# Performance work log

Measured on AMD Instinct MI355X. Metric: run time of the kernel, lower is better.

## Reference

```python
import jax, jax.numpy as jnp
import numpy as np

INPUT_SIZE = 64
HIDDEN = 128


def setup_inputs() -> dict:
    key = jax.random.key(0)
    ks = jax.random.split(key, 10)
    B, T, I, H = 512, 1024, INPUT_SIZE, HIDDEN
    s_ih = 1.0 / np.sqrt(H)
    inp = {
        "x": jax.random.normal(ks[0], (B, T, I), dtype=jnp.float32),
        # PyTorch nn.LSTM params, gate order (i, f, g, o)
        "W_ih": jax.random.uniform(ks[1], (4 * H, I), jnp.float32, -s_ih, s_ih),
        "W_hh": jax.random.uniform(ks[2], (4 * H, H), jnp.float32, -s_ih, s_ih),
        "b_ih": jax.random.uniform(ks[3], (4 * H,), jnp.float32, -s_ih, s_ih),
        "b_hh": jax.random.uniform(ks[4], (4 * H,), jnp.float32, -s_ih, s_ih),
        # fc1: 128 -> 256, fc2: 256 -> 1 (PyTorch Linear init bounds)
        "W1": jax.random.uniform(ks[5], (256, H), jnp.float32, -s_ih, s_ih),
        "b1": jax.random.uniform(ks[6], (256,), jnp.float32, -s_ih, s_ih),
        "W2": jax.random.uniform(ks[7], (1, 256), jnp.float32, -1.0 / 16, 1.0 / 16),
        "b2": jax.random.uniform(ks[8], (1,), jnp.float32, -1.0 / 16, 1.0 / 16),
    }
    return inp


def _lstm_last_hidden(x, W_ih, W_hh, b_ih, b_hh):
    B, T, I = x.shape
    H = W_hh.shape[1]
    # Precompute input projection for all timesteps in one big GEMM: [T, B, 4H]
    x_proj = jnp.einsum("bti,gi->tbg", x, W_ih) + (b_ih + b_hh)

    def step(carry, xp_t):
        h, c = carry
        gates = xp_t + h @ W_hh.T  # [B, 4H]
        i_g, f_g, g_g, o_g = jnp.split(gates, 4, axis=-1)
        i_g = jax.nn.sigmoid(i_g)
        f_g = jax.nn.sigmoid(f_g)
        g_g = jnp.tanh(g_g)
        o_g = jax.nn.sigmoid(o_g)
        c = f_g * c + i_g * g_g
        h = o_g * jnp.tanh(c)
        return (h, c), None

    h0 = jnp.zeros((B, H), dtype=x.dtype)
    c0 = jnp.zeros((B, H), dtype=x.dtype)
    (h_T, _), _ = jax.lax.scan(step, (h0, c0), x_proj)
    return h_T  # [B, H], equals output at last timestep


def reference(x, W_ih, W_hh, b_ih, b_hh, W1, b1, W2, b2):
    h_last = _lstm_last_hidden(x, W_ih, W_hh, b_ih, b_hh)  # x[:, -1, :] of LSTM outputs
    y = h_last @ W1.T + b1   # fc1 (no activation in original)
    y = y @ W2.T + b2        # fc2 -> [B, 1]
    return y
```

## Files before the change

### kernel.cpp

```cpp
#include <hip/hip_runtime.h>


#define T_STEPS 1024
#define ISZ 64
#define HSZ 128
#define ZSZ (ISZ + HSZ)
#define G4 512
#define BCHUNK 2
#define NTH 512
#define CLEN 48
#define NGATE 4

__device__ __forceinline__ float fast_sigmoid(float x) {
    return 1.0f / (1.0f + __expf(-x));
}

__device__ __forceinline__ float fast_tanh(float x) {
    float xc = fminf(fmaxf(x, -15.0f), 15.0f);
    float u = __expf(2.0f * xc);
    return (u - 1.0f) / (u + 1.0f);
}

__device__ __forceinline__ float quad_reduce(float v) {
    int t = __builtin_amdgcn_mov_dpp(__float_as_int(v), 0xB1, 0xF, 0xF, true);
    v += __int_as_float(t);
    t = __builtin_amdgcn_mov_dpp(__float_as_int(v), 0x4E, 0xF, 0xF, true);
    v += __int_as_float(t);
    return v;
}

__global__ __launch_bounds__(NTH, 2)
void lstm_fused_kernel(const float* __restrict__ x,
                       const float* __restrict__ W_ih,
                       const float* __restrict__ W_hh,
                       const float* __restrict__ b_ih,
                       const float* __restrict__ b_hh,
                       const float* __restrict__ W1,
                       const float* __restrict__ b1,
                       const float* __restrict__ W2,
                       const float* __restrict__ b2,
                       float* __restrict__ out)
{
    __shared__ __align__(16) float zbuf[BCHUNK][ZSZ];
    __shared__ __align__(16) float gbuf[BCHUNK][G4];
    __shared__ float red[BCHUNK][4];

    const int tid = threadIdx.x;
    const int b0 = blockIdx.x * BCHUNK;
    const int c  = tid & 3;
    const int qg = tid >> 2;

    float wt[NGATE][CLEN];
    #pragma unroll
    for (int i = 0; i < NGATE; ++i) {
        const int g = qg * 4 + i;
        const float* pih = W_ih + (size_t)g * ISZ;
        const float* phh = W_hh + (size_t)g * HSZ;
        #pragma unroll
        for (int k = 0; k < CLEN; ++k) {
            const int col = c * CLEN + k;
            const float* p = (col < ISZ) ? (pih + col) : (phh + (col - ISZ));
            wt[i][k] = *p;
        }
    }
    const float bias = b_ih[tid] + b_hh[tid];

    if (tid < BCHUNK * HSZ) zbuf[tid >> 7][ISZ + (tid & 127)] = 0.0f;
    if (tid >= 256 && tid < 256 + BCHUNK * ISZ) {
        int l = tid - 256;
        zbuf[l >> 6][l & 63] =
            x[((size_t)(b0 + (l >> 6)) * T_STEPS + 0) * ISZ + (l & 63)];
    }
    float c0 = 0.0f, c1 = 0.0f;
    __syncthreads();

    const int gsel = tid >> 7;

    for (int t = 0; t < T_STEPS; ++t) {
        float xpre = 0.0f;
        const bool pf = (tid >= 128) && (tid < 256) && (t + 1 < T_STEPS);
        if (pf) {
            int l = tid - 128;
            xpre = x[((size_t)(b0 + (l >> 6)) * T_STEPS + (t + 1)) * ISZ + (l & 63)];
        }

        float a[NGATE][2];
        #pragma unroll
        for (int i = 0; i < NGATE; ++i) { a[i][0] = 0.0f; a[i][1] = 0.0f; }
        {
            const float4* z0 = reinterpret_cast<const float4*>(zbuf[0]) + c * (CLEN / 4);
            const float4* z1 = reinterpret_cast<const float4*>(zbuf[1]) + c * (CLEN / 4);
            #pragma unroll
            for (int k = 0; k < CLEN / 4; ++k) {
                float4 u = z0[k];
                float4 v = z1[k];
                #pragma unroll
                for (int i = 0; i < NGATE; ++i) {
                    a[i][0] = fmaf(wt[i][4*k  ], u.x, a[i][0]);
                    a[i][0] = fmaf(wt[i][4*k+1], u.y, a[i][0]);
                    a[i][0] = fmaf(wt[i][4*k+2], u.z, a[i][0]);
                    a[i][0] = fmaf(wt[i][4*k+3], u.w, a[i][0]);
                    a[i][1] = fmaf(wt[i][4*k  ], v.x, a[i][1]);
                    a[i][1] = fmaf(wt[i][4*k+1], v.y, a[i][1]);
                    a[i][1] = fmaf(wt[i][4*k+2], v.z, a[i][1]);
                    a[i][1] = fmaf(wt[i][4*k+3], v.w, a[i][1]);
                }
            }
        }

        #pragma unroll
        for (int i = 0; i < NGATE; ++i) {
            a[i][0] = quad_reduce(a[i][0]);
            a[i][1] = quad_reduce(a[i][1]);
        }
        float s0 = (c == 0) ? a[0][0] : (c == 1) ? a[1][0] : (c == 2) ? a[2][0] : a[3][0];
        float s1 = (c == 0) ? a[0][1] : (c == 1) ? a[1][1] : (c == 2) ? a[2][1] : a[3][1];
        s0 += bias;
        s1 += bias;

        float v0, v1;
        if (gsel == 2) { v0 = fast_tanh(s0);    v1 = fast_tanh(s1);    }
        else           { v0 = fast_sigmoid(s0); v1 = fast_sigmoid(s1); }
        gbuf[0][tid] = v0;
        gbuf[1][tid] = v1;
        __syncthreads();

        if (tid < HSZ) {
            {
                float ig = gbuf[0][tid];
                float fg = gbuf[0][tid + 128];
                float gv = gbuf[0][tid + 256];
                float og = gbuf[0][tid + 384];
                c0 = fmaf(fg, c0, ig * gv);
                zbuf[0][ISZ + tid] = og * fast_tanh(c0);
            }
            {
                float ig = gbuf[1][tid];
                float fg = gbuf[1][tid + 128];
                float gv = gbuf[1][tid + 256];
                float og = gbuf[1][tid + 384];
                c1 = fmaf(fg, c1, ig * gv);
                zbuf[1][ISZ + tid] = og * fast_tanh(c1);
            }
        } else if (pf) {
            int l = tid - 128;
            zbuf[l >> 6][l & 63] = xpre;
        }
        __syncthreads();
    }

    {
        const int b = tid >> 8;
        const int m = tid & 255;
        const float4* w1r = reinterpret_cast<const float4*>(W1 + (size_t)m * HSZ);
        const float4* hr = reinterpret_cast<const float4*>(zbuf[b] + ISZ);
        float acc = 0.0f;
        #pragma unroll
        for (int k = 0; k < HSZ / 4; ++k) {
            float4 w = w1r[k];
            float4 h = hr[k];
            acc = fmaf(w.x, h.x, acc);
            acc = fmaf(w.y, h.y, acc);
            acc = fmaf(w.z, h.z, acc);
            acc = fmaf(w.w, h.w, acc);
        }
        float z = (acc + b1[m]) * W2[m];
        #pragma unroll
        for (int off = 32; off >= 1; off >>= 1)
            z += __shfl_down(z, off, 64);
        if ((tid & 63) == 0) red[b][(tid >> 6) & 3] = z;
    }
    __syncthreads();
    if (tid == 0)   out[b0]     = red[0][0] + red[0][1] + red[0][2] + red[0][3] + b2[0];
    if (tid == 256) out[b0 + 1] = red[1][0] + red[1][1] + red[1][2] + red[1][3] + b2[0];
}

extern "C" void kernel_launch(void* const* d_in, const int* in_sizes, int n_in,
                              void* d_out, int out_size, void* d_ws, size_t ws_size,
                              hipStream_t stream) {
    const float* x    = (const float*)d_in[0];
    const float* W_ih = (const float*)d_in[1];
    const float* W_hh = (const float*)d_in[2];
    const float* b_ih = (const float*)d_in[3];
    const float* b_hh = (const float*)d_in[4];
    const float* W1   = (const float*)d_in[5];
    const float* b1   = (const float*)d_in[6];
    const float* W2   = (const float*)d_in[7];
    const float* b2   = (const float*)d_in[8];
    float* out = (float*)d_out;

    lstm_fused_kernel<<<dim3(512 / BCHUNK), dim3(NTH), 0, stream>>>(
        x, W_ih, W_hh, b_ih, b_hh, W1, b1, W2, b2, out);
}
```

Before: 1.757 ms.

## Double threads per block and split dot products across eight lanes with butterfly reduction

Raises the block to 1024 threads so each gate row's 192-wide dot product is split across 8 lanes (24 weights each) instead of 4 (48 each). The cross-lane reduction becomes a reduce-scatter using a ds_swizzle xor-4 step plus DPP xor-2 and xor-1 steps, leaving each lane one final gate value for one batch row. The cell update is spread over 256 threads so each handles one batch row, instead of 128 threads each handling two. This halves the per-thread serial FMA chain and the register-held weights per step, at the cost of more waves per block, a slower swizzle step, and heavier per-step barrier synchronisation.

```diff
diff --git a/kernel.cpp b/kernel.cpp
--- a/kernel.cpp
+++ b/kernel.cpp
@@ -7,8 +7,8 @@
 #define ZSZ (ISZ + HSZ)
 #define G4 512
 #define BCHUNK 2
-#define NTH 512
-#define CLEN 48
+#define NTH 1024
+#define CLEN 24
 #define NGATE 4
 
 __device__ __forceinline__ float fast_sigmoid(float x) {
@@ -21,15 +21,17 @@
     return (u - 1.0f) / (u + 1.0f);
 }
 
-__device__ __forceinline__ float quad_reduce(float v) {
-    int t = __builtin_amdgcn_mov_dpp(__float_as_int(v), 0xB1, 0xF, 0xF, true);
-    v += __int_as_float(t);
-    t = __builtin_amdgcn_mov_dpp(__float_as_int(v), 0x4E, 0xF, 0xF, true);
-    v += __int_as_float(t);
-    return v;
+__device__ __forceinline__ float dpp_xor1(float v) {
+    return __int_as_float(__builtin_amdgcn_mov_dpp(__float_as_int(v), 0xB1, 0xF, 0xF, true));
+}
+__device__ __forceinline__ float dpp_xor2(float v) {
+    return __int_as_float(__builtin_amdgcn_mov_dpp(__float_as_int(v), 0x4E, 0xF, 0xF, true));
+}
+__device__ __forceinline__ float swz_xor4(float v) {
+    return __int_as_float(__builtin_amdgcn_ds_swizzle(__float_as_int(v), 0x101F));
 }
 
-__global__ __launch_bounds__(NTH, 2)
+__global__ __launch_bounds__(NTH, 4)
 void lstm_fused_kernel(const float* __restrict__ x,
                        const float* __restrict__ W_ih,
                        const float* __restrict__ W_hh,
@@ -47,23 +49,26 @@
 
     const int tid = threadIdx.x;
     const int b0 = blockIdx.x * BCHUNK;
-    const int c  = tid & 3;
-    const int qg = tid >> 2;
+    const int c  = tid & 7;
+    const int qg = tid >> 3;
+
+    const int g_own = 4 * qg + (c & 3);
+    const bool hi4 = (c & 4) != 0;
+    const bool hi2 = (c & 2) != 0;
+    const bool hi1 = (c & 1) != 0;
 
     float wt[NGATE][CLEN];
     #pragma unroll
     for (int i = 0; i < NGATE; ++i) {
-        const int g = qg * 4 + i;
-        const float* pih = W_ih + (size_t)g * ISZ;
-        const float* phh = W_hh + (size_t)g * HSZ;
+        const float* rih = W_ih + (size_t)(4 * qg + i) * ISZ;
+        const float* rhh = W_hh + (size_t)(4 * qg + i) * HSZ;
         #pragma unroll
         for (int k = 0; k < CLEN; ++k) {
             const int col = c * CLEN + k;
-            const float* p = (col < ISZ) ? (pih + col) : (phh + (col - ISZ));
-            wt[i][k] = *p;
+            wt[i][k] = (col < ISZ) ? rih[col] : rhh[col - ISZ];
         }
     }
-    const float bias = b_ih[tid] + b_hh[tid];
+    const float bias = b_ih[g_own] + b_hh[g_own];
 
     if (tid < BCHUNK * HSZ) zbuf[tid >> 7][ISZ + (tid & 127)] = 0.0f;
     if (tid >= 256 && tid < 256 + BCHUNK * ISZ) {
@@ -71,85 +76,83 @@
         zbuf[l >> 6][l & 63] =
             x[((size_t)(b0 + (l >> 6)) * T_STEPS + 0) * ISZ + (l & 63)];
     }
-    float c0 = 0.0f, c1 = 0.0f;
+    float cst = 0.0f;
     __syncthreads();
 
-    const int gsel = tid >> 7;
+    const int gsel = tid >> 8;
 
     for (int t = 0; t < T_STEPS; ++t) {
         float xpre = 0.0f;
-        const bool pf = (tid >= 128) && (tid < 256) && (t + 1 < T_STEPS);
+        const bool pf = (tid >= 512) && (tid < 640) && (t + 1 < T_STEPS);
         if (pf) {
-            int l = tid - 128;
+            int l = tid - 512;
             xpre = x[((size_t)(b0 + (l >> 6)) * T_STEPS + (t + 1)) * ISZ + (l & 63)];
         }
 
         float a[NGATE][2];
         #pragma unroll
         for (int i = 0; i < NGATE; ++i) { a[i][0] = 0.0f; a[i][1] = 0.0f; }
-        {
-            const float4* z0 = reinterpret_cast<const float4*>(zbuf[0]) + c * (CLEN / 4);
-            const float4* z1 = reinterpret_cast<const float4*>(zbuf[1]) + c * (CLEN / 4);
+        #pragma unroll
+        for (int r = 0; r < BCHUNK; ++r) {
+            const float4* zr = reinterpret_cast<const float4*>(zbuf[r]) + c * (CLEN / 4);
             #pragma unroll
             for (int k = 0; k < CLEN / 4; ++k) {
-                float4 u = z0[k];
-                float4 v = z1[k];
+                float4 u = zr[k];
                 #pragma unroll
                 for (int i = 0; i < NGATE; ++i) {
-                    a[i][0] = fmaf(wt[i][4*k  ], u.x, a[i][0]);
-                    a[i][0] = fmaf(wt[i][4*k+1], u.y, a[i][0]);
-                    a[i][0] = fmaf(wt[i][4*k+2], u.z, a[i][0]);
-                    a[i][0] = fmaf(wt[i][4*k+3], u.w, a[i][0]);
-                    a[i][1] = fmaf(wt[i][4*k  ], v.x, a[i][1]);
-                    a[i][1] = fmaf(wt[i][4*k+1], v.y, a[i][1]);
-                    a[i][1] = fmaf(wt[i][4*k+2], v.z, a[i][1]);
-                    a[i][1] = fmaf(wt[i][4*k+3], v.w, a[i][1]);
+                    a[i][r] = fmaf(wt[i][4*k  ], u.x, a[i][r]);
+                    a[i][r] = fmaf(wt[i][4*k+1], u.y, a[i][r]);
+                    a[i][r] = fmaf(wt[i][4*k+2], u.z, a[i][r]);
+                    a[i][r] = fmaf(wt[i][4*k+3], u.w, a[i][r]);
                 }
             }
         }
 
+        float g4[NGATE];
         #pragma unroll
         for (int i = 0; i < NGATE; ++i) {
-            a[i][0] = quad_reduce(a[i][0]);
-            a[i][1] = quad_reduce(a[i][1]);
+            float keep = hi4 ? a[i][1] : a[i][0];
+            float send = hi4 ? a[i][0] : a[i][1];
+            g4[i] = keep + swz_xor4(send);
         }
-        float s0 = (c == 0) ? a[0][0] : (c == 1) ? a[1][0] : (c == 2) ? a[2][0] : a[3][0];
-        float s1 = (c == 0) ? a[0][1] : (c == 1) ? a[1][1] : (c == 2) ? a[2][1] : a[3][1];
-        s0 += bias;
-        s1 += bias;
+        float g2[2];
+        {
+            float k0 = hi2 ? g4[2] : g4[0];
+            float s0 = hi2 ? g4[0] : g4[2];
+            float k1 = hi2 ? g4[3] : g4[1];
+            float s1 = hi2 ? g4[1] : g4[3];
+            g2[0] = k0 + dpp_xor2(s0);
+            g2[1] = k1 + dpp_xor2(s1);
+        }
+        float s;
+        {
+            float kc = hi1 ? g2[1] : g2[0];
+            float sc = hi1 ? g2[0] : g2[1];
+            s = kc + dpp_xor1(sc);
+        }
+        s += bias;
 
-        float v0, v1;
-        if (gsel == 2) { v0 = fast_tanh(s0);    v1 = fast_tanh(s1);    }
-        else           { v0 = fast_sigmoid(s0); v1 = fast_sigmoid(s1); }
-        gbuf[0][tid] = v0;
-        gbuf[1][tid] = v1;
+        float v = (gsel == 2) ? fast_tanh(s) : fast_sigmoid(s);
+        gbuf[c >> 2][g_own] = v;
         __syncthreads();
 
-        if (tid < HSZ) {
-            {
-                float ig = gbuf[0][tid];
-                float fg = gbuf[0][tid + 128];
-                float gv = gbuf[0][tid + 256];
-                float og = gbuf[0][tid + 384];
-                c0 = fmaf(fg, c0, ig * gv);
-                zbuf[0][ISZ + tid] = og * fast_tanh(c0);
-            }
-            {
-                float ig = gbuf[1][tid];
-                float fg = gbuf[1][tid + 128];
-                float gv = gbuf[1][tid + 256];
-                float og = gbuf[1][tid + 384];
-                c1 = fmaf(fg, c1, ig * gv);
-                zbuf[1][ISZ + tid] = og * fast_tanh(c1);
-            }
+        if (tid < BCHUNK * HSZ) {
+            const int r = tid >> 7;
+            const int j = tid & 127;
+            float ig = gbuf[r][j];
+            float fg = gbuf[r][j + 128];
+            float gv = gbuf[r][j + 256];
+            float og = gbuf[r][j + 384];
+            cst = fmaf(fg, cst, ig * gv);
+            zbuf[r][ISZ + j] = og * fast_tanh(cst);
         } else if (pf) {
-            int l = tid - 128;
+            int l = tid - 512;
             zbuf[l >> 6][l & 63] = xpre;
         }
         __syncthreads();
     }
 
-    {
+    if (tid < 512) {
         const int b = tid >> 8;
         const int m = tid & 255;
         const float4* w1r = reinterpret_cast<const float4*>(W1 + (size_t)m * HSZ);
```

Result: faster. 1.583 ms (-9.9%).
